# Optimization experiments

Hardware: AMD Instinct MI355X
Metric: run time of the kernel (lower is better)

Reference implementation:

```python
import jax, jax.numpy as jnp
import numpy as np
import math

B, S, D = 8, 2048, 512
X_SCALE = 0.02  # keep exp(x @ x^T) finite (raw unit-variance dots ~N(0, D) would overflow exp)


def setup_inputs() -> dict:
    key = jax.random.key(0)
    kx, km = jax.random.split(key)
    x = jax.random.normal(kx, (B, S, D), dtype=jnp.float32) * X_SCALE
    mask = jax.random.randint(km, (B, S, S), 0, 2, dtype=jnp.int32)
    return {"x": x, "mask": mask}


def reference(x, mask):
    # scores = exp(x @ x^T) / sqrt(D)  -- non-standard: exp BEFORE scaling/softmax
    scores = jnp.exp(jnp.einsum("bqd,bkd->bqk", x, x)) / math.sqrt(x.shape[-1])
    scores = jnp.where(mask == 0, jnp.float32(-1e9), scores)
    p_attn = jax.nn.softmax(scores, axis=-1)  # dropout is identity in eval mode
    output = jnp.einsum("bqk,bkd->bqd", p_attn, x)
    # flatten=True path: sum over sequence dim
    return output.sum(axis=1), p_attn
```

## Files before the change

kernel.cpp:

```cpp
#include <hip/hip_runtime.h>
#include <cstdint>
#include <cstddef>

#define B_ 8
#define S_ 2048
#define D_ 512

typedef __attribute__((ext_vector_type(8))) short short8;
typedef __attribute__((ext_vector_type(4))) float f32x4;

__device__ inline unsigned short f2bf(float f) {
  unsigned u = __float_as_uint(f);
  u += 0x7FFFu + ((u >> 16) & 1u);
  return (unsigned short)(u >> 16);
}

__global__ void convert_kernel(const float* __restrict__ x,
                               unsigned short* __restrict__ xb, int n4) {
  const float4* x4 = (const float4*)x;
  ushort4* o4 = (ushort4*)xb;
  for (int i = blockIdx.x * blockDim.x + threadIdx.x; i < n4;
       i += gridDim.x * blockDim.x) {
    float4 v = x4[i];
    ushort4 o;
    o.x = f2bf(v.x); o.y = f2bf(v.y); o.z = f2bf(v.z); o.w = f2bf(v.w);
    o4[i] = o;
  }
}

__global__ void pack_mask_kernel(const int* __restrict__ mask,
                                 unsigned char* __restrict__ bm, int nbytes) {
  for (int j = blockIdx.x * blockDim.x + threadIdx.x; j < nbytes;
       j += gridDim.x * blockDim.x) {
    const int4* m4 = (const int4*)mask + 2 * (size_t)j;
    int4 a = m4[0], b = m4[1];
    unsigned byte = (unsigned)(a.x != 0) | ((unsigned)(a.y != 0) << 1) |
                    ((unsigned)(a.z != 0) << 2) | ((unsigned)(a.w != 0) << 3) |
                    ((unsigned)(b.x != 0) << 4) | ((unsigned)(b.y != 0) << 5) |
                    ((unsigned)(b.z != 0) << 6) | ((unsigned)(b.w != 0) << 7);
    bm[j] = (unsigned char)byte;
  }
}

#define GLDS(g, l) __builtin_amdgcn_global_load_lds( \
    (const __attribute__((address_space(1))) void*)(g), \
    (__attribute__((address_space(3))) void*)(l), 16, 0, 0)

template <bool WRITE_P>
__global__ __launch_bounds__(256) void gemm_pass(
    const unsigned short* __restrict__ xb, const unsigned char* __restrict__ bm,
    float* __restrict__ pbuf, float* __restrict__ Z, float* __restrict__ cs) {
  __shared__ unsigned short At[128 * 64];
  __shared__ unsigned short Bt[128 * 64];
  __shared__ unsigned char mrow[128 * 16];
  __shared__ float zl[128];

  const int b = blockIdx.z;
  const int qt = blockIdx.y;
  const int kt = blockIdx.x;
  const int tid = threadIdx.x;
  const int wid = tid >> 6;
  const int lane = tid & 63;
  const int l15 = lane & 15;
  const int l7 = lane & 7;
  const int lg = lane >> 4;

  const unsigned short* xbat = xb + (size_t)b * S_ * D_;
  const unsigned short* aglob = xbat + (size_t)qt * 128 * D_;
  const unsigned short* bglob = xbat + (size_t)kt * 128 * D_;

  if (tid < 128) {
    *(uint4*)&mrow[tid * 16] =
        *(const uint4*)(bm + ((size_t)b * S_ + qt * 128 + tid) * (S_ / 8) +
                        kt * 16);
    if (WRITE_P) zl[tid] = 1.0f / Z[b * S_ + qt * 128 + tid];
  }

  f32x4 acc[4][4] = {};

  const int wr = (wid >> 1) * 64;
  const int wc = (wid & 1) * 64;

  for (int k0 = 0; k0 < D_; k0 += 64) {
    __syncthreads();
    #pragma unroll
    for (int i = 0; i < 4; i++) {
      int c = i * 256 + tid;
      int row = c >> 3;
      int col8 = (c & 7) ^ (row & 7);
      GLDS(aglob + row * D_ + k0 + col8 * 8, &At[c * 8]);
      GLDS(bglob + row * D_ + k0 + col8 * 8, &Bt[c * 8]);
    }
    __syncthreads();
    #pragma unroll
    for (int ks8 = 0; ks8 < 8; ks8 += 4) {
      const int kc8 = ks8 + lg;
      short8 av[4], bv[4];
      #pragma unroll
      for (int m = 0; m < 4; m++) {
        int row = wr + m * 16 + l15;
        av[m] = *(const short8*)&At[row * 64 + ((kc8 ^ l7) << 3)];
      }
      #pragma unroll
      for (int n = 0; n < 4; n++) {
        int row = wc + n * 16 + l15;
        bv[n] = *(const short8*)&Bt[row * 64 + ((kc8 ^ l7) << 3)];
      }
      #pragma unroll
      for (int m = 0; m < 4; m++)
        #pragma unroll
        for (int n = 0; n < 4; n++)
          acc[m][n] = __builtin_amdgcn_mfma_f32_16x16x32_bf16(
              av[m], bv[n], acc[m][n], 0, 0, 0);
    }
  }
  __syncthreads();

  const float inv_sqrt_d = 0.04419417382415922f;
  float* pbat = pbuf + (size_t)b * S_ * S_;
  float* Zb = Z + b * S_;
  float* csb = cs + b * S_;
  float csum[4] = {0.f, 0.f, 0.f, 0.f};

  #pragma unroll
  for (int m = 0; m < 4; m++) {
    float rsum[4] = {0.f, 0.f, 0.f, 0.f};
    #pragma unroll
    for (int r = 0; r < 4; r++) {
      const int trow = wr + m * 16 + lg * 4 + r;
      const uint2 mb = *(const uint2*)&mrow[trow * 16 + (wc >> 3)];
      const float zinv = WRITE_P ? zl[trow] : 0.f;
      #pragma unroll
      for (int n = 0; n < 4; n++) {
        const int idx = n * 16 + l15;
        const unsigned bit =
            (n < 2) ? (mb.x >> idx) : (mb.y >> (idx - 32));
        float u = 0.0f;
        if (bit & 1u)
          u = __expf(__expf(acc[m][n][r]) * inv_sqrt_d);
        if (WRITE_P) {
          float p = u * zinv;
          pbat[(size_t)(qt * 128 + trow) * S_ + kt * 128 + wc + n * 16 + l15] = p;
          csum[n] += p;
        } else {
          rsum[r] += u;
        }
      }
    }
    if (!WRITE_P) {
      #pragma unroll
      for (int r = 0; r < 4; r++) {
        float v = rsum[r];
        v += __shfl_xor(v, 1);
        v += __shfl_xor(v, 2);
        v += __shfl_xor(v, 4);
        v += __shfl_xor(v, 8);
        if (l15 == 0)
          atomicAdd(&Zb[qt * 128 + wr + m * 16 + lg * 4 + r], v);
      }
    }
  }
  if (WRITE_P) {
    #pragma unroll
    for (int n = 0; n < 4; n++) {
      float v = csum[n];
      v += __shfl_xor(v, 16);
      v += __shfl_xor(v, 32);
      if (lg == 0)
        atomicAdd(&csb[kt * 128 + wc + n * 16 + l15], v);
    }
  }
}

__global__ __launch_bounds__(512) void out_kernel(
    const float* __restrict__ x, const float* __restrict__ cs,
    float* __restrict__ out) {
  const int b = blockIdx.y;
  const int k0 = blockIdx.x * 128;
  const int d = threadIdx.x;
  const float* xbat = x + (size_t)b * S_ * D_;
  const float* csb = cs + b * S_;
  float acc = 0.f;
  for (int k = k0; k < k0 + 128; k++)
    acc += csb[k] * xbat[(size_t)k * D_ + d];
  atomicAdd(&out[b * D_ + d], acc);
}

extern "C" void kernel_launch(void* const* d_in, const int* in_sizes, int n_in,
                              void* d_out, int out_size, void* d_ws, size_t ws_size,
                              hipStream_t stream) {
  const float* x = (const float*)d_in[0];
  const int* mask = (const int*)d_in[1];
  float* out = (float*)d_out;
  float* p = out + B_ * D_;

  unsigned short* xb = (unsigned short*)d_ws;
  unsigned char* bm = (unsigned char*)d_ws + (size_t)B_ * S_ * D_ * 2;
  float* Z = (float*)(bm + (size_t)B_ * S_ * (S_ / 8));
  float* cs = Z + B_ * S_;

  hipMemsetAsync(Z, 0, 2 * (size_t)B_ * S_ * sizeof(float), stream);
  hipMemsetAsync(out, 0, (size_t)B_ * D_ * sizeof(float), stream);

  convert_kernel<<<2048, 256, 0, stream>>>(x, xb, B_ * S_ * D_ / 4);
  pack_mask_kernel<<<2048, 256, 0, stream>>>(mask, bm, B_ * S_ * (S_ / 8));
  gemm_pass<false><<<dim3(S_ / 128, S_ / 128, B_), 256, 0, stream>>>(
      xb, bm, p, Z, cs);
  gemm_pass<true><<<dim3(S_ / 128, S_ / 128, B_), 256, 0, stream>>>(
      xb, bm, p, Z, cs);
  out_kernel<<<dim3(S_ / 128, B_), 512, 0, stream>>>(x, cs, out);
}
```

Baseline: 382.6 us.

## Replace second GEMM pass with unnormalized write plus separate normalize kernel

Rather than running the score GEMM twice (once to get row sums Z, once to write normalized P), a single GEMM pass now writes the unnormalized exp scores to the output buffer and accumulates Z. A separate streaming kernel then rescales P by 1/Z and accumulates the column sums. It also fuses the convert and mask-pack kernels, remaps block indices so tiles of one batch spread across XCDs, and splits out_kernel into more blocks. The trade is removing a full GEMM recompute at the cost of an extra read and write pass over the 128MB P matrix.

Result: faster. 374.1 us (-2.2%).

```diff
diff --git a/kernel.cpp b/kernel.cpp
--- a/kernel.cpp
+++ b/kernel.cpp
@@ -15,23 +15,20 @@
   return (unsigned short)(u >> 16);
 }
 
-__global__ void convert_kernel(const float* __restrict__ x,
-                               unsigned short* __restrict__ xb, int n4) {
+__global__ __launch_bounds__(256) void prep_kernel(
+    const float* __restrict__ x, unsigned short* __restrict__ xb,
+    const int* __restrict__ mask, unsigned char* __restrict__ bm) {
+  const int tid = blockIdx.x * blockDim.x + threadIdx.x;
+  const int nth = gridDim.x * blockDim.x;
   const float4* x4 = (const float4*)x;
   ushort4* o4 = (ushort4*)xb;
-  for (int i = blockIdx.x * blockDim.x + threadIdx.x; i < n4;
-       i += gridDim.x * blockDim.x) {
+  for (int i = tid; i < B_ * S_ * D_ / 4; i += nth) {
     float4 v = x4[i];
     ushort4 o;
     o.x = f2bf(v.x); o.y = f2bf(v.y); o.z = f2bf(v.z); o.w = f2bf(v.w);
     o4[i] = o;
   }
-}
-
-__global__ void pack_mask_kernel(const int* __restrict__ mask,
-                                 unsigned char* __restrict__ bm, int nbytes) {
-  for (int j = blockIdx.x * blockDim.x + threadIdx.x; j < nbytes;
-       j += gridDim.x * blockDim.x) {
+  for (int j = tid; j < B_ * S_ * S_ / 8; j += nth) {
     const int4* m4 = (const int4*)mask + 2 * (size_t)j;
     int4 a = m4[0], b = m4[1];
     unsigned byte = (unsigned)(a.x != 0) | ((unsigned)(a.y != 0) << 1) |
@@ -46,18 +43,17 @@
     (const __attribute__((address_space(1))) void*)(g), \
     (__attribute__((address_space(3))) void*)(l), 16, 0, 0)
 
-template <bool WRITE_P>
-__global__ __launch_bounds__(256) void gemm_pass(
+__global__ __launch_bounds__(256) void gemm_u_kernel(
     const unsigned short* __restrict__ xb, const unsigned char* __restrict__ bm,
-    float* __restrict__ pbuf, float* __restrict__ Z, float* __restrict__ cs) {
+    float* __restrict__ ubuf, float* __restrict__ Z) {
   __shared__ unsigned short At[128 * 64];
   __shared__ unsigned short Bt[128 * 64];
   __shared__ unsigned char mrow[128 * 16];
-  __shared__ float zl[128];
-
-  const int b = blockIdx.z;
-  const int qt = blockIdx.y;
-  const int kt = blockIdx.x;
+
+  const int logical = (blockIdx.x & 7) * 256 + (blockIdx.x >> 3);
+  const int b = logical >> 8;
+  const int qt = (logical >> 4) & 15;
+  const int kt = logical & 15;
   const int tid = threadIdx.x;
   const int wid = tid >> 6;
   const int lane = tid & 63;
@@ -73,7 +69,6 @@
     *(uint4*)&mrow[tid * 16] =
         *(const uint4*)(bm + ((size_t)b * S_ + qt * 128 + tid) * (S_ / 8) +
                         kt * 16);
-    if (WRITE_P) zl[tid] = 1.0f / Z[b * S_ + qt * 128 + tid];
   }
 
   f32x4 acc[4][4] = {};
@@ -117,10 +112,8 @@
   __syncthreads();
 
   const float inv_sqrt_d = 0.04419417382415922f;
-  float* pbat = pbuf + (size_t)b * S_ * S_;
+  float* ubat = ubuf + (size_t)b * S_ * S_;
   float* Zb = Z + b * S_;
-  float* csb = cs + b * S_;
-  float csum[4] = {0.f, 0.f, 0.f, 0.f};
 
   #pragma unroll
   for (int m = 0; m < 4; m++) {
@@ -129,59 +122,72 @@
     for (int r = 0; r < 4; r++) {
       const int trow = wr + m * 16 + lg * 4 + r;
       const uint2 mb = *(const uint2*)&mrow[trow * 16 + (wc >> 3)];
-      const float zinv = WRITE_P ? zl[trow] : 0.f;
       #pragma unroll
       for (int n = 0; n < 4; n++) {
         const int idx = n * 16 + l15;
-        const unsigned bit =
-            (n < 2) ? (mb.x >> idx) : (mb.y >> (idx - 32));
+        const unsigned bit = (n < 2) ? (mb.x >> idx) : (mb.y >> (idx - 32));
         float u = 0.0f;
         if (bit & 1u)
           u = __expf(__expf(acc[m][n][r]) * inv_sqrt_d);
-        if (WRITE_P) {
-          float p = u * zinv;
-          pbat[(size_t)(qt * 128 + trow) * S_ + kt * 128 + wc + n * 16 + l15] = p;
-          csum[n] += p;
-        } else {
-          rsum[r] += u;
-        }
+        ubat[(size_t)(qt * 128 + trow) * S_ + kt * 128 + wc + n * 16 + l15] = u;
+        rsum[r] += u;
       }
     }
-    if (!WRITE_P) {
-      #pragma unroll
-      for (int r = 0; r < 4; r++) {
-        float v = rsum[r];
-        v += __shfl_xor(v, 1);
-        v += __shfl_xor(v, 2);
-        v += __shfl_xor(v, 4);
-        v += __shfl_xor(v, 8);
-        if (l15 == 0)
-          atomicAdd(&Zb[qt * 128 + wr + m * 16 + lg * 4 + r], v);
-      }
-    }
-  }
-  if (WRITE_P) {
-    #pragma unroll
-    for (int n = 0; n < 4; n++) {
-      float v = csum[n];
-      v += __shfl_xor(v, 16);
-      v += __shfl_xor(v, 32);
-      if (lg == 0)
-        atomicAdd(&csb[kt * 128 + wc + n * 16 + l15], v);
-    }
-  }
+    #pragma unroll
+    for (int r = 0; r < 4; r++) {
+      float v = rsum[r];
+      v += __shfl_xor(v, 1);
+      v += __shfl_xor(v, 2);
+      v += __shfl_xor(v, 4);
+      v += __shfl_xor(v, 8);
+      if (l15 == 0)
+        atomicAdd(&Zb[qt * 128 + wr + m * 16 + lg * 4 + r], v);
+    }
+  }
+}
+
+__global__ __launch_bounds__(256) void norm_kernel(
+    float* __restrict__ p, const float* __restrict__ Z, float* __restrict__ cs) {
+  const int b = blockIdx.y;
+  const int qc = blockIdx.x;
+  const int t = threadIdx.x;
+  float4* prow = (float4*)(p + ((size_t)b * S_ + qc * 16) * S_);
+  const float* Zb = Z + b * S_ + qc * 16;
+  float4 a0 = {0.f, 0.f, 0.f, 0.f};
+  float4 a1 = {0.f, 0.f, 0.f, 0.f};
+  for (int r = 0; r < 16; r++) {
+    float invZ = 1.0f / Zb[r];
+    float4 u0 = prow[r * 512 + t];
+    float4 u1 = prow[r * 512 + t + 256];
+    u0.x *= invZ; u0.y *= invZ; u0.z *= invZ; u0.w *= invZ;
+    u1.x *= invZ; u1.y *= invZ; u1.z *= invZ; u1.w *= invZ;
+    prow[r * 512 + t] = u0;
+    prow[r * 512 + t + 256] = u1;
+    a0.x += u0.x; a0.y += u0.y; a0.z += u0.z; a0.w += u0.w;
+    a1.x += u1.x; a1.y += u1.y; a1.z += u1.z; a1.w += u1.w;
+  }
+  float* csb = cs + b * S_;
+  atomicAdd(&csb[4 * t + 0], a0.x);
+  atomicAdd(&csb[4 * t + 1], a0.y);
+  atomicAdd(&csb[4 * t + 2], a0.z);
+  atomicAdd(&csb[4 * t + 3], a0.w);
+  atomicAdd(&csb[1024 + 4 * t + 0], a1.x);
+  atomicAdd(&csb[1024 + 4 * t + 1], a1.y);
+  atomicAdd(&csb[1024 + 4 * t + 2], a1.z);
+  atomicAdd(&csb[1024 + 4 * t + 3], a1.w);
 }
 
 __global__ __launch_bounds__(512) void out_kernel(
     const float* __restrict__ x, const float* __restrict__ cs,
     float* __restrict__ out) {
   const int b = blockIdx.y;
-  const int k0 = blockIdx.x * 128;
+  const int k0 = blockIdx.x * 32;
   const int d = threadIdx.x;
   const float* xbat = x + (size_t)b * S_ * D_;
   const float* csb = cs + b * S_;
   float acc = 0.f;
-  for (int k = k0; k < k0 + 128; k++)
+  #pragma unroll 8
+  for (int k = k0; k < k0 + 32; k++)
     acc += csb[k] * xbat[(size_t)k * D_ + d];
   atomicAdd(&out[b * D_ + d], acc);
 }
@@ -202,11 +208,8 @@
   hipMemsetAsync(Z, 0, 2 * (size_t)B_ * S_ * sizeof(float), stream);
   hipMemsetAsync(out, 0, (size_t)B_ * D_ * sizeof(float), stream);
 
-  convert_kernel<<<2048, 256, 0, stream>>>(x, xb, B_ * S_ * D_ / 4);
-  pack_mask_kernel<<<2048, 256, 0, stream>>>(mask, bm, B_ * S_ * (S_ / 8));
-  gemm_pass<false><<<dim3(S_ / 128, S_ / 128, B_), 256, 0, stream>>>(
-      xb, bm, p, Z, cs);
-  gemm_pass<true><<<dim3(S_ / 128, S_ / 128, B_), 256, 0, stream>>>(
-      xb, bm, p, Z, cs);
-  out_kernel<<<dim3(S_ / 128, B_), 512, 0, stream>>>(x, cs, out);
-}
+  prep_kernel<<<2048, 256, 0, stream>>>(x, xb, mask, bm);
+  gemm_u_kernel<<<2048, 256, 0, stream>>>(xb, bm, p, Z);
+  norm_kernel<<<dim3(S_ / 16, B_), 256, 0, stream>>>(p, Z, cs);
+  out_kernel<<<dim3(S_ / 32, B_), 512, 0, stream>>>(x, cs, out);
+}
```
